# Kernel optimization log

Measured on AMD Instinct MI355X. Metric: run time of the kernel, lower is better.

## Reference

```python
import jax, jax.numpy as jnp
import numpy as np

COUPLING = 0.12
EPS = 1e-08
EMBED_DIM = 16
H = 4
REL_MAX_DIST = 64
PAST_LEN = 524288


def setup_inputs() -> dict:
    key = jax.random.key(0)
    ks = jax.random.split(key, 7)
    return {
        "candidate": jax.random.normal(ks[0], (EMBED_DIM, 2), dtype=jnp.float32),
        "z_past": jax.random.normal(ks[1], (PAST_LEN, EMBED_DIM, 2), dtype=jnp.float32),
        "heads_w": jax.random.normal(ks[2], (H, 2 * EMBED_DIM, 4 * EMBED_DIM), dtype=jnp.float32) * 0.05,
        "heads_b": jax.random.normal(ks[3], (H, 2 * EMBED_DIM), dtype=jnp.float32) * 0.05,
        "out_w": jax.random.normal(ks[4], (2 * EMBED_DIM, H * 2 * EMBED_DIM), dtype=jnp.float32) * 0.05,
        "out_b": jax.random.normal(ks[5], (2 * EMBED_DIM,), dtype=jnp.float32) * 0.05,
        "rel_bias": jax.random.normal(ks[6], (2 * REL_MAX_DIST + 1, 2), dtype=jnp.float32) * 0.02,
        "norm_scale": jnp.ones((1,), dtype=jnp.float32),
        "pos": PAST_LEN,
    }


def reference(candidate, z_past, heads_w, heads_b, out_w, out_b, rel_bias, norm_scale, pos):
    # candidate: [D,2] (real/imag), z_past: [P,D,2]
    P, D = z_past.shape[0], z_past.shape[1]
    # features_c = cat([z_curr_rep, z_past], -1); view_as_real + flatten -> [P, 4D]
    feats = jnp.concatenate(
        [jnp.broadcast_to(candidate[None], (P, D, 2)), z_past], axis=1
    ).reshape(P, 4 * D)
    # 4 small MLP heads, tanh, concat: [P, H, 2D] -> mean over past -> [H*2D]
    h = jnp.tanh(jnp.einsum("pd,hod->pho", feats, heads_w) + heads_b[None])
    combined_mean = h.reshape(P, -1).mean(axis=0)
    out = out_w @ combined_mean + out_b          # [2D]
    mod = out.reshape(D, 2)                      # complex mod as real/imag pair
    # relative positional bias: mean over gathered (clipped) indices
    rel = jnp.arange(pos - P, pos)
    idx = jnp.clip(rel + REL_MAX_DIST, 0, 2 * REL_MAX_DIST)
    bias_mean = rel_bias[idx].mean(axis=0)       # [2]
    # z_new = candidate + COUPLING * (mod + bias_mean)
    z = candidate + COUPLING * (mod + bias_mean[None, :])
    # tanh applied independently to real and imag parts
    z = jnp.tanh(z)
    max_int = jnp.max(jnp.sum(z * z, axis=-1))   # max |z|^2
    scale = norm_scale[0] / jnp.sqrt(max_int + EPS)
    return jnp.where(max_int > 0, z * scale, z)  # [D,2]
```

## Files before the change

### kernel.cpp

```cpp
#include <hip/hip_runtime.h>
#include <hip/hip_bf16.h>
#include <math.h>

#define COUPLING 0.12f
#define EPSV 1e-8f
#define SCALE2L2E 2.8853900817779268f

typedef __attribute__((ext_vector_type(8))) short bf16x8;
typedef __attribute__((ext_vector_type(4))) float f32x4;

__device__ __forceinline__ float tanh_from_e2(float y) {
    float e = __builtin_amdgcn_exp2f(y);
    float r = __builtin_amdgcn_rcpf(1.0f + e);
    return fmaf(-2.0f, r, 1.0f);
}
__device__ __forceinline__ float tanh_fast(float x) {
    return tanh_from_e2(SCALE2L2E * x);
}
__device__ __forceinline__ float sig_e2(float y) {
    float e = __builtin_amdgcn_exp2f(y);
    return __builtin_amdgcn_rcpf(1.0f + e);
}

__device__ __forceinline__ short f2bf(float f) {
    __hip_bfloat16 h = __float2bfloat16(f);
    return __builtin_bit_cast(short, h);
}

__global__ __launch_bounds__(128) void phot_prep(
    const float* __restrict__ heads_w, const float* __restrict__ heads_b,
    const float* __restrict__ cand, float* __restrict__ cpre,
    short* __restrict__ wbf)
{
    const int oh = threadIdx.x;
    const float* wr = heads_w + (size_t)oh * 64;
    float s0 = heads_b[oh], s1 = 0.f, s2 = 0.f, s3 = 0.f;
    #pragma unroll
    for (int k = 0; k < 32; k += 4) {
        s0 = fmaf(wr[k+0], cand[k+0], s0);
        s1 = fmaf(wr[k+1], cand[k+1], s1);
        s2 = fmaf(wr[k+2], cand[k+2], s2);
        s3 = fmaf(wr[k+3], cand[k+3], s3);
    }
    cpre[oh] = SCALE2L2E * ((s0 + s1) + (s2 + s3));
    short* wo = wbf + (size_t)oh * 32;
    #pragma unroll
    for (int k = 0; k < 32; ++k) wo[k] = f2bf(SCALE2L2E * wr[32 + k]);
}

__global__ __launch_bounds__(256, 8) void phot_main(
    const float* __restrict__ z_past,
    const short* __restrict__ wbf,
    const float* __restrict__ cpre_g,
    float* __restrict__ partials,
    int P, int NB)
{
    __shared__ float wacc[128];
    __shared__ __align__(16) unsigned short zb[2][512];

    const int tid  = threadIdx.x;
    const int lane = tid & 63;
    const int wv   = tid >> 6;
    const int col  = lane & 15;
    const int kg   = lane >> 4;

    const int g0 = wv * 2, g1 = g0 + 1;
    const bf16x8 bfA = *(const bf16x8*)(wbf + (size_t)(g0 * 16 + col) * 32 + kg * 8);
    const bf16x8 bfB = *(const bf16x8*)(wbf + (size_t)(g1 * 16 + col) * 32 + kg * 8);
    const float  cpA = cpre_g[g0 * 16 + col];
    const float  cpB = cpre_g[g1 * 16 + col];

    f32x4 accA = {0,0,0,0}, accB = {0,0,0,0};

    const int T  = (P + 15) >> 4;
    const int Tf = P >> 4;
    const int b  = blockIdx.x;
    const int K  = (b < T) ? ((T - 1 - b) / NB + 1) : 0;

    const int a_off = col * 64 + ((kg ^ ((col >> 1) & 3)) << 4);

    const int f0   = (wv << 7) + (lane << 1);
    const int srow = f0 >> 5;
    const int scol = f0 & 31;
    const int w_off = srow * 64 + ((((scol >> 3) ^ ((srow >> 1) & 3))) << 4)
                    + ((scol & 7) << 1);

    float2 pre;
    #define SLOAD(tt) { \
        int tc = (tt); if (tc > T - 1) tc = T - 1; \
        int grow = tc * 16 + srow; if (grow > P - 1) grow = P - 1; \
        pre = *(const float2*)(z_past + (size_t)grow * 32 + scol); }
    #define SWRITE(bi) { \
        unsigned int pk = ((unsigned int)(unsigned short)f2bf(pre.y) << 16) | \
                          (unsigned int)(unsigned short)f2bf(pre.x); \
        *(unsigned int*)((char*)&zb[(bi)][0] + w_off) = pk; }

    if (K > 0) {
        SLOAD(b);
        SWRITE(0);
        SLOAD(b + NB);
        __syncthreads();

        for (int k = 0; k < K; ++k) {
            const int tt = b + k * NB;
            const bf16x8 a = *(const bf16x8*)((const char*)&zb[k & 1][0] + a_off);

            if (k + 1 < K) SWRITE((k + 1) & 1);
            SLOAD(b + (k + 2) * NB);

            const int base = tt * 16;
            if (base + 16 <= P) {
                f32x4 c = {cpA, cpA, cpA, cpA};
                f32x4 d = __builtin_amdgcn_mfma_f32_16x16x32_bf16(a, bfA, c, 0, 0, 0);
                accA[0] += sig_e2(d[0]); accA[1] += sig_e2(d[1]);
                accA[2] += sig_e2(d[2]); accA[3] += sig_e2(d[3]);
                c = {cpB, cpB, cpB, cpB};
                d = __builtin_amdgcn_mfma_f32_16x16x32_bf16(a, bfB, c, 0, 0, 0);
                accB[0] += sig_e2(d[0]); accB[1] += sig_e2(d[1]);
                accB[2] += sig_e2(d[2]); accB[3] += sig_e2(d[3]);
            } else {
                const int r0 = base + kg * 4;
                f32x4 c = {cpA, cpA, cpA, cpA};
                f32x4 d = __builtin_amdgcn_mfma_f32_16x16x32_bf16(a, bfA, c, 0, 0, 0);
                if (r0 + 0 < P) accA[0] += sig_e2(d[0]);
                if (r0 + 1 < P) accA[1] += sig_e2(d[1]);
                if (r0 + 2 < P) accA[2] += sig_e2(d[2]);
                if (r0 + 3 < P) accA[3] += sig_e2(d[3]);
                c = {cpB, cpB, cpB, cpB};
                d = __builtin_amdgcn_mfma_f32_16x16x32_bf16(a, bfB, c, 0, 0, 0);
                if (r0 + 0 < P) accB[0] += sig_e2(d[0]);
                if (r0 + 1 < P) accB[1] += sig_e2(d[1]);
                if (r0 + 2 < P) accB[2] += sig_e2(d[2]);
                if (r0 + 3 < P) accB[3] += sig_e2(d[3]);
            }
            __syncthreads();
        }
    }
    #undef SLOAD
    #undef SWRITE

    float nsum = 0.0f;
    if (K > 0) {
        int nfull = (b < Tf) ? ((Tf - 1 - b) / NB + 1) : 0;
        nsum = 4.0f * (float)nfull;
        if (Tf < T && b <= Tf && ((Tf - b) % NB) == 0) {
            int prem = P - Tf * 16;
            int nv = prem - kg * 4; if (nv < 0) nv = 0; if (nv > 4) nv = 4;
            nsum += (float)nv;
        }
    }

    float sA = nsum - 2.0f * ((accA[0] + accA[1]) + (accA[2] + accA[3]));
    sA += __shfl_xor(sA, 16, 64);
    sA += __shfl_xor(sA, 32, 64);
    float sB = nsum - 2.0f * ((accB[0] + accB[1]) + (accB[2] + accB[3]));
    sB += __shfl_xor(sB, 16, 64);
    sB += __shfl_xor(sB, 32, 64);
    if (lane < 16) {
        wacc[g0 * 16 + lane] = sA;
        wacc[g1 * 16 + lane] = sB;
    }
    __syncthreads();
    if (tid < 128) {
        partials[(size_t)b * 128 + tid] = wacc[tid];
    }
}

__global__ __launch_bounds__(1024) void phot_finalize(
    const float* __restrict__ partials, int nblk, int P,
    const float* __restrict__ out_w,
    const float* __restrict__ out_b,
    const float* __restrict__ rel_bias,
    const float* __restrict__ cand,
    const float* __restrict__ norm_scale,
    const int* __restrict__ posp,
    float* __restrict__ out)
{
    __shared__ float  sh[1024];
    __shared__ float  cm[128];
    __shared__ float  outv[32];
    __shared__ double db[512];
    __shared__ float  bm[2];

    const int t  = threadIdx.x;
    const int oh = t & 127;
    const int sl = t >> 7;

    const int seg = nblk >> 3;
    const int b0  = sl * seg;
    float a0=0.f,a1=0.f,a2=0.f,a3=0.f,a4=0.f,a5=0.f,a6=0.f,a7=0.f;
    int i = 0;
    for (; i + 8 <= seg; i += 8) {
        const float* pp = partials + (size_t)(b0 + i) * 128 + oh;
        a0 += pp[0*128]; a1 += pp[1*128]; a2 += pp[2*128]; a3 += pp[3*128];
        a4 += pp[4*128]; a5 += pp[5*128]; a6 += pp[6*128]; a7 += pp[7*128];
    }
    for (; i < seg; ++i) a0 += partials[(size_t)(b0 + i) * 128 + oh];
    sh[t] = ((a0+a1)+(a2+a3)) + ((a4+a5)+(a6+a7));
    __syncthreads();

    if (t < 128) {
        float s = 0.0f;
        #pragma unroll
        for (int s2 = 0; s2 < 8; ++s2) s += sh[t + 128*s2];
        cm[t] = s / (float)P;
    }

    if (t < 512) {
        const int c = t >> 8, j = t & 255;
        double v = 0.0;
        if (j <= 128) {
            const long long pos = (long long)(*posp);
            const long long a = pos - (long long)P + 64;
            double cnt;
            if (j == 0) {
                long long hi = -a; if (hi > (long long)P - 1) hi = (long long)P - 1;
                cnt = (hi >= 0) ? (double)(hi + 1) : 0.0;
            } else if (j == 128) {
                long long lo = 128 - a; if (lo < 0) lo = 0;
                cnt = (lo <= (long long)P - 1) ? (double)((long long)P - lo) : 0.0;
            } else {
                long long p = (long long)j - a;
                cnt = (p >= 0 && p < (long long)P) ? 1.0 : 0.0;
            }
            v = cnt * (double)rel_bias[2*j + c];
        }
        db[t] = v;
    }
    __syncthreads();
    #pragma unroll
    for (int s = 128; s >= 1; s >>= 1) {
        if (t < 512 && (t & 255) < s) db[t] += db[t + s];
        __syncthreads();
    }
    if (t < 2) bm[t] = (float)(db[t << 8] / (double)P);
    __syncthreads();

    if (t < 32) {
        const float* wr = out_w + t * 128;
        float o0 = out_b[t], o1 = 0.f, o2 = 0.f, o3 = 0.f;
        #pragma unroll
        for (int j = 0; j < 128; j += 4) {
            o0 = fmaf(wr[j+0], cm[j+0], o0);
            o1 = fmaf(wr[j+1], cm[j+1], o1);
            o2 = fmaf(wr[j+2], cm[j+2], o2);
            o3 = fmaf(wr[j+3], cm[j+3], o3);
        }
        outv[t] = (o0+o1) + (o2+o3);
    }
    __syncthreads();

    if (t < 32) {
        float zt = tanh_fast(cand[t] + COUPLING * (outv[t] + bm[t & 1]));
        float other = __shfl_xor(zt, 1, 64);
        float m = fmaf(zt, zt, other * other);
        #pragma unroll
        for (int off = 2; off < 32; off <<= 1) m = fmaxf(m, __shfl_xor(m, off, 64));
        float scale = norm_scale[0] / sqrtf(m + EPSV);
        out[t] = (m > 0.0f) ? zt * scale : zt;
    }
}

extern "C" void kernel_launch(void* const* d_in, const int* in_sizes, int n_in,
                              void* d_out, int out_size, void* d_ws, size_t ws_size,
                              hipStream_t stream)
{
    const float* cand       = (const float*)d_in[0];
    const float* z_past     = (const float*)d_in[1];
    const float* heads_w    = (const float*)d_in[2];
    const float* heads_b    = (const float*)d_in[3];
    const float* out_w      = (const float*)d_in[4];
    const float* out_b      = (const float*)d_in[5];
    const float* rel_bias   = (const float*)d_in[6];
    const float* norm_scale = (const float*)d_in[7];
    const int*   posp       = (const int*)d_in[8];

    const int P = in_sizes[1] / 32;

    int nblk = 2048;
    size_t need = ((size_t)nblk * 128 + 128) * sizeof(float) + 128 * 32 * sizeof(short);
    if (need > ws_size) {
        nblk = (int)((ws_size - 128 * sizeof(float) - 128 * 32 * sizeof(short))
                     / (128 * sizeof(float)));
        nblk &= ~7;
        if (nblk < 8) nblk = 8;
    }
    float* partials = (float*)d_ws;
    float* cpre     = partials + (size_t)nblk * 128;
    short* wbf      = (short*)(cpre + 128);

    phot_prep<<<1, 128, 0, stream>>>(heads_w, heads_b, cand, cpre, wbf);
    phot_main<<<nblk, 256, 0, stream>>>(z_past, wbf, cpre, partials, P, nblk);
    phot_finalize<<<1, 1024, 0, stream>>>(partials, nblk, P, out_w, out_b,
                                          rel_bias, cand, norm_scale, posp,
                                          (float*)d_out);
}
```

Measured before the change: 42.81 us.

## Batch four tiles per barrier with wider loads and add two-stage partial reduction

The main loop now has each wave load a full 16-row tile with 32-byte vector loads, stage four tiles per phase in a triple-buffered LDS ring, and have every wave compute all four tiles before one barrier. This cuts barriers per tile and widens global loads to reduce sync and latency overhead. A new phot_mid kernel reduces the 2048 per-block partials into 128 rows in parallel, so the single-block finalize has less serial work. The cost is an extra kernel launch and more LDS per block, which could lower occupancy.

```diff
diff --git a/kernel.cpp b/kernel.cpp
--- a/kernel.cpp
+++ b/kernel.cpp
@@ -56,7 +56,7 @@
     int P, int NB)
 {
     __shared__ float wacc[128];
-    __shared__ __align__(16) unsigned short zb[2][512];
+    __shared__ __align__(16) unsigned short zb[3][4][512];
 
     const int tid  = threadIdx.x;
     const int lane = tid & 63;
@@ -76,68 +76,83 @@
     const int Tf = P >> 4;
     const int b  = blockIdx.x;
     const int K  = (b < T) ? ((T - 1 - b) / NB + 1) : 0;
-
-    const int a_off = col * 64 + ((kg ^ ((col >> 1) & 3)) << 4);
-
-    const int f0   = (wv << 7) + (lane << 1);
-    const int srow = f0 >> 5;
-    const int scol = f0 & 31;
-    const int w_off = srow * 64 + ((((scol >> 3) ^ ((srow >> 1) & 3))) << 4)
-                    + ((scol & 7) << 1);
-
-    float2 pre;
-    #define SLOAD(tt) { \
-        int tc = (tt); if (tc > T - 1) tc = T - 1; \
-        int grow = tc * 16 + srow; if (grow > P - 1) grow = P - 1; \
-        pre = *(const float2*)(z_past + (size_t)grow * 32 + scol); }
-    #define SWRITE(bi) { \
-        unsigned int pk = ((unsigned int)(unsigned short)f2bf(pre.y) << 16) | \
-                          (unsigned int)(unsigned short)f2bf(pre.x); \
-        *(unsigned int*)((char*)&zb[(bi)][0] + w_off) = pk; }
+    const int PH = (K + 3) >> 2;
+
+    const int sr = lane >> 2;
+    const int sc = lane & 3;
+    const int woff = sr * 32 + ((sc ^ (sr & 3)) << 3);
+
+    const int roff = col * 32 + ((kg ^ (col & 3)) << 3);
+
+    f32x4 preA, preB;
+
+    #define SLOADP(ph) { \
+        const int j_ = 4 * (ph) + wv; \
+        if (j_ < K) { \
+            const int tt_ = b + j_ * NB; \
+            int grow = tt_ * 16 + sr; if (grow > P - 1) grow = P - 1; \
+            const float* g_ = z_past + (size_t)grow * 32 + sc * 8; \
+            preA = *(const f32x4*)g_; \
+            preB = *(const f32x4*)(g_ + 4); \
+        } }
+    #define SWRITEP(ph) { \
+        const int j_ = 4 * (ph) + wv; \
+        if (j_ < K) { \
+            bf16x8 w_; \
+            w_[0]=f2bf(preA[0]); w_[1]=f2bf(preA[1]); w_[2]=f2bf(preA[2]); w_[3]=f2bf(preA[3]); \
+            w_[4]=f2bf(preB[0]); w_[5]=f2bf(preB[1]); w_[6]=f2bf(preB[2]); w_[7]=f2bf(preB[3]); \
+            *(bf16x8*)(&zb[(ph) % 3][wv][woff]) = w_; \
+        } }
+    #define CTILE(p, j) { \
+        const int jj_ = 4 * (p) + (j); \
+        if (jj_ < K) { \
+            const int tt_ = b + jj_ * NB; \
+            const bf16x8 a_ = *(const bf16x8*)(&zb[(p) % 3][j][roff]); \
+            const int base_ = tt_ * 16; \
+            if (base_ + 16 <= P) { \
+                f32x4 c_ = {cpA, cpA, cpA, cpA}; \
+                f32x4 d_ = __builtin_amdgcn_mfma_f32_16x16x32_bf16(a_, bfA, c_, 0, 0, 0); \
+                accA[0] += sig_e2(d_[0]); accA[1] += sig_e2(d_[1]); \
+                accA[2] += sig_e2(d_[2]); accA[3] += sig_e2(d_[3]); \
+                c_ = {cpB, cpB, cpB, cpB}; \
+                d_ = __builtin_amdgcn_mfma_f32_16x16x32_bf16(a_, bfB, c_, 0, 0, 0); \
+                accB[0] += sig_e2(d_[0]); accB[1] += sig_e2(d_[1]); \
+                accB[2] += sig_e2(d_[2]); accB[3] += sig_e2(d_[3]); \
+            } else { \
+                const int r0_ = base_ + kg * 4; \
+                f32x4 c_ = {cpA, cpA, cpA, cpA}; \
+                f32x4 d_ = __builtin_amdgcn_mfma_f32_16x16x32_bf16(a_, bfA, c_, 0, 0, 0); \
+                if (r0_ + 0 < P) accA[0] += sig_e2(d_[0]); \
+                if (r0_ + 1 < P) accA[1] += sig_e2(d_[1]); \
+                if (r0_ + 2 < P) accA[2] += sig_e2(d_[2]); \
+                if (r0_ + 3 < P) accA[3] += sig_e2(d_[3]); \
+                c_ = {cpB, cpB, cpB, cpB}; \
+                d_ = __builtin_amdgcn_mfma_f32_16x16x32_bf16(a_, bfB, c_, 0, 0, 0); \
+                if (r0_ + 0 < P) accB[0] += sig_e2(d_[0]); \
+                if (r0_ + 1 < P) accB[1] += sig_e2(d_[1]); \
+                if (r0_ + 2 < P) accB[2] += sig_e2(d_[2]); \
+                if (r0_ + 3 < P) accB[3] += sig_e2(d_[3]); \
+            } \
+        } }
 
     if (K > 0) {
-        SLOAD(b);
-        SWRITE(0);
-        SLOAD(b + NB);
-        __syncthreads();
-
-        for (int k = 0; k < K; ++k) {
-            const int tt = b + k * NB;
-            const bf16x8 a = *(const bf16x8*)((const char*)&zb[k & 1][0] + a_off);
-
-            if (k + 1 < K) SWRITE((k + 1) & 1);
-            SLOAD(b + (k + 2) * NB);
-
-            const int base = tt * 16;
-            if (base + 16 <= P) {
-                f32x4 c = {cpA, cpA, cpA, cpA};
-                f32x4 d = __builtin_amdgcn_mfma_f32_16x16x32_bf16(a, bfA, c, 0, 0, 0);
-                accA[0] += sig_e2(d[0]); accA[1] += sig_e2(d[1]);
-                accA[2] += sig_e2(d[2]); accA[3] += sig_e2(d[3]);
-                c = {cpB, cpB, cpB, cpB};
-                d = __builtin_amdgcn_mfma_f32_16x16x32_bf16(a, bfB, c, 0, 0, 0);
-                accB[0] += sig_e2(d[0]); accB[1] += sig_e2(d[1]);
-                accB[2] += sig_e2(d[2]); accB[3] += sig_e2(d[3]);
-            } else {
-                const int r0 = base + kg * 4;
-                f32x4 c = {cpA, cpA, cpA, cpA};
-                f32x4 d = __builtin_amdgcn_mfma_f32_16x16x32_bf16(a, bfA, c, 0, 0, 0);
-                if (r0 + 0 < P) accA[0] += sig_e2(d[0]);
-                if (r0 + 1 < P) accA[1] += sig_e2(d[1]);
-                if (r0 + 2 < P) accA[2] += sig_e2(d[2]);
-                if (r0 + 3 < P) accA[3] += sig_e2(d[3]);
-                c = {cpB, cpB, cpB, cpB};
-                d = __builtin_amdgcn_mfma_f32_16x16x32_bf16(a, bfB, c, 0, 0, 0);
-                if (r0 + 0 < P) accB[0] += sig_e2(d[0]);
-                if (r0 + 1 < P) accB[1] += sig_e2(d[1]);
-                if (r0 + 2 < P) accB[2] += sig_e2(d[2]);
-                if (r0 + 3 < P) accB[3] += sig_e2(d[3]);
-            }
-            __syncthreads();
+        SLOADP(0);
+        SWRITEP(0);
+        SLOADP(1);
+        asm volatile("s_waitcnt lgkmcnt(0)" ::: "memory");
+        __builtin_amdgcn_s_barrier();
+
+        for (int p = 0; p < PH; ++p) {
+            if (p + 1 < PH) SWRITEP(p + 1);
+            if (p + 2 < PH) SLOADP(p + 2);
+            CTILE(p, 0); CTILE(p, 1); CTILE(p, 2); CTILE(p, 3);
+            asm volatile("s_waitcnt lgkmcnt(0)" ::: "memory");
+            __builtin_amdgcn_s_barrier();
         }
     }
-    #undef SLOAD
-    #undef SWRITE
+    #undef SLOADP
+    #undef SWRITEP
+    #undef CTILE
 
     float nsum = 0.0f;
     if (K > 0) {
@@ -164,6 +179,19 @@
     if (tid < 128) {
         partials[(size_t)b * 128 + tid] = wacc[tid];
     }
+}
+
+__global__ __launch_bounds__(128) void phot_mid(
+    const float* __restrict__ partials, float* __restrict__ mid, int nblk)
+{
+    const int g = blockIdx.x, t = threadIdx.x;
+    const int seg = nblk >> 7, rem = nblk & 127;
+    const int b0  = g * seg + (g < rem ? g : rem);
+    const int cnt = seg + (g < rem ? 1 : 0);
+    const float* p0 = partials + (size_t)b0 * 128 + t;
+    float s = 0.f;
+    for (int i = 0; i < cnt; ++i) s += p0[(size_t)i * 128];
+    mid[(size_t)g * 128 + t] = s;
 }
 
 __global__ __launch_bounds__(1024) void phot_finalize(
@@ -278,20 +306,23 @@
     const int P = in_sizes[1] / 32;
 
     int nblk = 2048;
-    size_t need = ((size_t)nblk * 128 + 128) * sizeof(float) + 128 * 32 * sizeof(short);
+    size_t need = ((size_t)nblk * 128 + 128 * 128 + 128) * sizeof(float)
+                + 128 * 32 * sizeof(short);
     if (need > ws_size) {
-        nblk = (int)((ws_size - 128 * sizeof(float) - 128 * 32 * sizeof(short))
-                     / (128 * sizeof(float)));
+        nblk = (int)((ws_size - (128 * 128 + 128) * sizeof(float)
+                      - 128 * 32 * sizeof(short)) / (128 * sizeof(float)));
         nblk &= ~7;
         if (nblk < 8) nblk = 8;
     }
     float* partials = (float*)d_ws;
-    float* cpre     = partials + (size_t)nblk * 128;
+    float* mid      = partials + (size_t)nblk * 128;
+    float* cpre     = mid + 128 * 128;
     short* wbf      = (short*)(cpre + 128);
 
     phot_prep<<<1, 128, 0, stream>>>(heads_w, heads_b, cand, cpre, wbf);
     phot_main<<<nblk, 256, 0, stream>>>(z_past, wbf, cpre, partials, P, nblk);
-    phot_finalize<<<1, 1024, 0, stream>>>(partials, nblk, P, out_w, out_b,
+    phot_mid<<<128, 128, 0, stream>>>(partials, mid, nblk);
+    phot_finalize<<<1, 1024, 0, stream>>>(mid, 128, P, out_w, out_b,
                                           rel_bias, cand, norm_scale, posp,
                                           (float*)d_out);
 }
```

New measurement: 39.00 us. 1.1x faster.
